# Kernel optimization log

Hardware: AMD Instinct MI355X
Metric: run time of the kernel (lower is better)

The kernel has to match this reference:

```python
import jax, jax.numpy as jnp
import numpy as np

B, S, D = 8, 1024, 1024
H, DH = 16, 64  # num_attention_heads, attention_head_size; H*DH == D


def setup_inputs() -> dict:
    key = jax.random.key(0)
    ks = jax.random.split(key, 6)
    scale = 0.02
    return {
        "hidden_states": jax.random.normal(ks[0], (B, S, D), jnp.float32),
        "right_hidden_states": jax.random.normal(ks[1], (B, S, D), jnp.float32),
        "attention_mask": jnp.ones((B, S, S), jnp.float32),
        "Wq": jax.random.normal(ks[2], (D, H * DH), jnp.float32) * scale,
        "bq": jnp.zeros((H * DH,), jnp.float32),
        "Wk": jax.random.normal(ks[3], (D, H * DH), jnp.float32) * scale,
        "bk": jnp.zeros((H * DH,), jnp.float32),
        "Wv": jax.random.normal(ks[4], (D, H * DH), jnp.float32) * scale,
        "bv": jnp.zeros((H * DH,), jnp.float32),
    }


def _split_heads(x, b):
    # (B, S, H*DH) -> (B, H, S, DH)
    return x.reshape(b, -1, H, DH).transpose(0, 2, 1, 3)


def reference(hidden_states, right_hidden_states, attention_mask, Wq, bq, Wk, bk, Wv, bv):
    b = hidden_states.shape[0]
    q = _split_heads(hidden_states @ Wq + bq, b)          # (B,H,Sq,DH)
    k = _split_heads(right_hidden_states @ Wk + bk, b)    # (B,H,Sk,DH)
    v = _split_heads(right_hidden_states @ Wv + bv, b)    # (B,H,Sk,DH)

    scores = jnp.einsum("bhqd,bhkd->bhqk", q, k) / jnp.sqrt(jnp.asarray(DH, q.dtype))
    scores = jnp.sum(scores, axis=1, keepdims=True)       # (B,1,Sq,Sk) head-summed

    ext = (1.0 - attention_mask[:, None, :, :].astype(scores.dtype)) * -1e9
    probs = jax.nn.softmax(scores + ext, axis=-1)         # (B,1,Sq,Sk)

    ctx = jnp.matmul(probs, v)                            # broadcast -> (B,H,Sq,DH)
    # Faithful to original: reshape WITHOUT transposing heads back.
    return ctx.reshape(b, -1, H * DH)                     # (B,Sq,H*DH)
```

## Files before the change

### kernel.cpp

```cpp
#include <hip/hip_runtime.h>
#include <stdint.h>

constexpr int S = 1024;
constexpr int D = 1024;
constexpr int NB = 8;

typedef __bf16 bf16x8 __attribute__((ext_vector_type(8)));
typedef float floatx4 __attribute__((ext_vector_type(4)));

#define AS1 __attribute__((address_space(1)))
#define AS3 __attribute__((address_space(3)))

__device__ __forceinline__ unsigned short f2bf(float f) {
  unsigned u = __builtin_bit_cast(unsigned, f);
  u += 0x7fffu + ((u >> 16) & 1u);
  return (unsigned short)(u >> 16);
}

__device__ __forceinline__ ushort4 f2bf4(float4 w) {
  ushort4 o;
  o.x = f2bf(w.x); o.y = f2bf(w.y); o.z = f2bf(w.z); o.w = f2bf(w.w);
  return o;
}

__device__ __forceinline__ void gload16(const void* g, void* l) {
  __builtin_amdgcn_global_load_lds((const AS1 unsigned int*)g, (AS3 unsigned int*)l, 16, 0, 0);
}

__global__ __launch_bounds__(256) void prep_kernel(
    const float4* __restrict__ hs4, const float4* __restrict__ rhs4,
    ushort4* __restrict__ hsb4, ushort4* __restrict__ rhsb4,
    const float* __restrict__ Wq, const float* __restrict__ Wk, const float* __restrict__ Wv,
    unsigned short* __restrict__ WvT, unsigned short* __restrict__ Mtb,
    const float* __restrict__ bq, const float* __restrict__ bk, float* __restrict__ u,
    float* __restrict__ v, float* __restrict__ cbuf) {
  __shared__ float tile[32][33];
  __shared__ float bsh[1024];
  __shared__ float sh[256];
  __shared__ int nz2;
  __shared__ __align__(16) unsigned short Am[64 * 32];
  __shared__ __align__(16) unsigned short Bm[64 * 32];
  const int bid = blockIdx.x;
  const int tid = threadIdx.x;
  if (bid < 256) {
    const int bx = bid & 15;
    const int by = bid >> 4;
    const int srow = tid >> 2;
    const int scg8 = (((tid & 3) ^ ((srow >> 1) & 3)) * 8);
    const int lw8 = (tid & 3) * 8;
    const float* aGp = Wk + (long long)(by * 64 + srow) * 1024 + scg8;
    const float* bGp = Wq + (long long)(bx * 64 + srow) * 1024 + scg8;
    const int lane = tid & 63;
    const int w4 = tid >> 6;
    const int r15 = lane & 15;
    const int quad = lane >> 4;
    const int pq = (quad ^ ((r15 >> 1) & 3)) * 8;
    const int wm2 = (w4 >> 1) * 32;
    const int wn2 = (w4 & 1) * 32;
    floatx4 acc[2][2];
    for (int i = 0; i < 2; ++i)
      for (int j = 0; j < 2; ++j) acc[i][j] = {0.f, 0.f, 0.f, 0.f};
    for (int k0 = 0; k0 < 1024; k0 += 32) {
      float4 a0 = *(const float4*)(aGp + k0);
      float4 a1 = *(const float4*)(aGp + k0 + 4);
      float4 b0 = *(const float4*)(bGp + k0);
      float4 b1 = *(const float4*)(bGp + k0 + 4);
      ushort4 ua0 = f2bf4(a0), ua1 = f2bf4(a1), ub0 = f2bf4(b0), ub1 = f2bf4(b1);
      __syncthreads();
      *(ushort4*)(Am + srow * 32 + lw8) = ua0;
      *(ushort4*)(Am + srow * 32 + lw8 + 4) = ua1;
      *(ushort4*)(Bm + srow * 32 + lw8) = ub0;
      *(ushort4*)(Bm + srow * 32 + lw8 + 4) = ub1;
      __syncthreads();
      bf16x8 af[2], bfr[2];
      for (int t = 0; t < 2; ++t) {
        af[t] = *reinterpret_cast<const bf16x8*>(Am + (wm2 + t * 16 + r15) * 32 + pq);
        bfr[t] = *reinterpret_cast<const bf16x8*>(Bm + (wn2 + t * 16 + r15) * 32 + pq);
      }
      for (int mt = 0; mt < 2; ++mt)
        for (int nt = 0; nt < 2; ++nt)
          acc[mt][nt] =
              __builtin_amdgcn_mfma_f32_16x16x32_bf16(af[mt], bfr[nt], acc[mt][nt], 0, 0, 0);
    }
    for (int mt = 0; mt < 2; ++mt)
      for (int nt = 0; nt < 2; ++nt) {
        const int mr = by * 64 + wm2 + mt * 16 + quad * 4;
        const int nc = bx * 64 + wn2 + nt * 16 + r15;
        floatx4 vv = acc[mt][nt];
        for (int e = 0; e < 4; ++e)
          Mtb[(long long)(mr + e) * 1024 + nc] = f2bf(vv[e] * 0.125f);
      }
  } else if (bid < 2304) {
    const int base = (bid - 256) * 256 + tid;
    float4 a0 = hs4[base];
    float4 a1 = hs4[base + 524288];
    float4 a2 = hs4[base + 1048576];
    float4 a3 = hs4[base + 1572864];
    float4 b0 = rhs4[base];
    float4 b1 = rhs4[base + 524288];
    float4 b2 = rhs4[base + 1048576];
    float4 b3 = rhs4[base + 1572864];
    hsb4[base] = f2bf4(a0);
    hsb4[base + 524288] = f2bf4(a1);
    hsb4[base + 1048576] = f2bf4(a2);
    hsb4[base + 1572864] = f2bf4(a3);
    rhsb4[base] = f2bf4(b0);
    rhsb4[base + 524288] = f2bf4(b1);
    rhsb4[base + 1048576] = f2bf4(b2);
    rhsb4[base + 1572864] = f2bf4(b3);
  } else if (bid < 3328) {
    const int r = bid - 2304;
    const int bx = (r & 31) * 32;
    const int by = (r >> 5) * 32;
    const int x = tid & 31;
    const int y0 = tid >> 5;
    for (int i = 0; i < 4; ++i) {
      int y = y0 + i * 8;
      tile[y][x] = Wv[(by + y) * D + bx + x];
    }
    __syncthreads();
    for (int i = 0; i < 4; ++i) {
      int y = y0 + i * 8;
      WvT[(long long)(bx + y) * D + by + x] = f2bf(tile[x][y]);
    }
  } else if (bid < 3336) {
    const bool isU = bid < 3332;
    const int blk = isU ? (bid - 3328) : (bid - 3332);
    const float* W = isU ? Wq : Wk;
    const float* bvec = isU ? bk : bq;
    float* outv = isU ? u : v;
    if (tid == 0) nz2 = 0;
    __syncthreads();
    float4 q = ((const float4*)bvec)[tid];
    bsh[tid * 4 + 0] = q.x;
    bsh[tid * 4 + 1] = q.y;
    bsh[tid * 4 + 2] = q.z;
    bsh[tid * 4 + 3] = q.w;
    if (q.x != 0.f || q.y != 0.f || q.z != 0.f || q.w != 0.f) nz2 = 1;
    __syncthreads();
    const int row0 = blk * 256;
    if (!nz2) {
      outv[row0 + tid] = 0.f;
      return;
    }
    const int lane = tid & 63;
    const int wv = tid >> 6;
    for (int rr = 0; rr < 64; ++rr) {
      const int row = row0 + wv * 64 + rr;
      const float* rp = W + (long long)row * 1024;
      float s = 0.f;
#pragma unroll
      for (int k = 0; k < 16; ++k) s += rp[lane + 64 * k] * bsh[lane + 64 * k];
      s += __shfl_xor(s, 32, 64);
      s += __shfl_xor(s, 16, 64);
      s += __shfl_xor(s, 8, 64);
      s += __shfl_xor(s, 4, 64);
      s += __shfl_xor(s, 2, 64);
      s += __shfl_xor(s, 1, 64);
      if (lane == 0) outv[row] = 0.125f * s;
    }
  } else {
    float s = 0.f;
    for (int c = tid; c < 1024; c += 256) s += bq[c] * bk[c];
    sh[tid] = s;
    __syncthreads();
    for (int o = 128; o; o >>= 1) {
      if (tid < o) sh[tid] += sh[tid + o];
      __syncthreads();
    }
    if (tid == 0) cbuf[0] = 0.125f * sh[0];
  }
}


#define GEMM_COMMON_IDX                  \
  const int tid = threadIdx.x;           \
  const int lane = tid & 63;             \
  const int w = tid >> 6;                \
  const int r15 = lane & 15;             \
  const int quad = lane >> 4;            \
  const int pq = (quad ^ ((r15 >> 1) & 3)) * 8; \
  const int wm = (w >> 1) * 64;          \
  const int wn = (w & 1) * 64;

#define GEMM_ACC_INIT                    \
  floatx4 acc[4][4];                     \
  for (int i = 0; i < 4; ++i)            \
    for (int j = 0; j < 4; ++j) acc[i][j] = {0.f, 0.f, 0.f, 0.f};

#define GEMM_STAGE_SETUP64(Abase, lda_, Bbase, ldb_)                          \
  const int srow = tid >> 2;                                                  \
  const int scg = (((tid & 3) ^ ((srow >> 1) & 3)) * 8);                      \
  const unsigned short* aG0 = (Abase) + (long long)srow * (lda_) + scg;       \
  const unsigned short* aG1 = aG0 + (long long)64 * (lda_);                   \
  const unsigned short* bG0 = (Bbase) + (long long)srow * (ldb_) + scg;       \
  const unsigned short* bG1 = bG0 + (long long)64 * (ldb_);

#define GEMM_KLOOP64(Klen)                                                               \
  for (int k0 = 0; k0 < (Klen); k0 += 64) {                                              \
    gload16(aG0 + k0, As[0] + w * 512);                                                  \
    gload16(aG1 + k0, As[0] + w * 512 + 2048);                                           \
    gload16(aG0 + k0 + 32, As[1] + w * 512);                                             \
    gload16(aG1 + k0 + 32, As[1] + w * 512 + 2048);                                      \
    gload16(bG0 + k0, Bs[0] + w * 512);                                                  \
    gload16(bG1 + k0, Bs[0] + w * 512 + 2048);                                           \
    gload16(bG0 + k0 + 32, Bs[1] + w * 512);                                             \
    gload16(bG1 + k0 + 32, Bs[1] + w * 512 + 2048);                                      \
    __syncthreads();                                                                     \
    for (int h = 0; h < 2; ++h) {                                                        \
      bf16x8 af[4], bfr[4];                                                              \
      for (int t = 0; t < 4; ++t) {                                                      \
        af[t] = *reinterpret_cast<const bf16x8*>(As[h] + (wm + t * 16 + r15) * 32 + pq); \
        bfr[t] = *reinterpret_cast<const bf16x8*>(Bs[h] + (wn + t * 16 + r15) * 32 + pq);\
      }                                                                                  \
      for (int mt = 0; mt < 4; ++mt)                                                     \
        for (int nt = 0; nt < 4; ++nt)                                                   \
          acc[mt][nt] =                                                                  \
              __builtin_amdgcn_mfma_f32_16x16x32_bf16(af[mt], bfr[nt], acc[mt][nt], 0, 0, 0); \
    }                                                                                    \
    __syncthreads();                                                                     \
  }

__global__ __launch_bounds__(256) void gemm_fused_kernel(
    const unsigned short* __restrict__ hsb, const unsigned short* __restrict__ rhsb,
    const unsigned short* __restrict__ Mtb, const unsigned short* __restrict__ WvT,
    const float* __restrict__ bv, unsigned short* __restrict__ hsMb,
    unsigned short* __restrict__ Vmt, const float* __restrict__ hs,
    const float* __restrict__ rhs, const float* __restrict__ u, const float* __restrict__ v,
    const float* __restrict__ cbuf, float* __restrict__ t2, float* __restrict__ t3) {
  __shared__ __align__(16) unsigned short As[2][4096];
  __shared__ __align__(16) unsigned short Bs[2][4096];
  GEMM_COMMON_IDX
  const int bid = blockIdx.x;
  if (bid >= 1024) {
    __shared__ int nz;
    const bool isT2 = bid < 1056;
    const int row = ((isT2 ? bid - 1024 : bid - 1056) << 8) + tid;
    const float* vec = isT2 ? u : v;
    const float* mat = isT2 ? hs : rhs;
    float* outp = isT2 ? t2 : t3;
    if (tid == 0) nz = 0;
    __syncthreads();
    float4 q = ((const float4*)vec)[tid];
    if (q.x != 0.f || q.y != 0.f || q.z != 0.f || q.w != 0.f) nz = 1;
    __syncthreads();
    const float c2 = 0.5f * cbuf[0];
    if (!nz) {
      outp[row] = c2;
      return;
    }
    const float4* r4 = (const float4*)(mat + (long long)row * 1024);
    float s = 0.f;
    for (int c4 = 0; c4 < 256; ++c4) {
      float4 h = r4[c4];
      s += h.x * vec[c4 * 4 + 0] + h.y * vec[c4 * 4 + 1] + h.z * vec[c4 * 4 + 2] +
           h.w * vec[c4 * 4 + 3];
    }
    outp[row] = s + c2;
    return;
  }
  const int swz = (bid & 7) * 128 + (bid >> 3);
  const int bx = swz & 15;
  const int by = swz >> 4;
  const int seg = bx >> 3;
  const long long nloc = (long long)(bx & 7) * 128;
  const long long m0 = (long long)by * 128;
  const unsigned short* A = ((seg == 0) ? hsb : rhsb) + m0 * D;
  const unsigned short* Bt = ((seg == 0) ? Mtb : WvT) + nloc * D;

  GEMM_STAGE_SETUP64(A, D, Bt, D)
  GEMM_ACC_INIT
  GEMM_KLOOP64(D)

  for (int mt = 0; mt < 4; ++mt) {
    for (int nt = 0; nt < 4; ++nt) {
      const long long mrow = m0 + wm + mt * 16 + quad * 4;
      const long long nc = nloc + wn + nt * 16 + r15;
      floatx4 vv = acc[mt][nt];
      if (seg == 0) {
        for (int e = 0; e < 4; ++e) hsMb[(mrow + e) * D + nc] = f2bf(vv[e]);
      } else {
        const float bval = bv[nc];
        for (int e = 0; e < 4; ++e) {
          long long m = mrow + e;
          Vmt[(m >> 10) * (long long)(S * D) + nc * S + (m & 1023)] = f2bf(vv[e] + bval);
        }
      }
    }
  }
}

__global__ __launch_bounds__(256) void gemm_scores_kernel(
    const unsigned short* __restrict__ hsMb, const unsigned short* __restrict__ rhsb,
    const float* __restrict__ mask, unsigned short* __restrict__ E, float* __restrict__ rowsumP,
    const float* __restrict__ t2, const float* __restrict__ t3) {
  __shared__ __align__(16) unsigned short As[2][4096];
  __shared__ __align__(16) unsigned short Bs[2][4096];
  GEMM_COMMON_IDX
  const int bid = blockIdx.x;
  const int z = bid & 7;
  const int r = bid >> 3;
  const int by = r >> 3;
  const int bx = r & 7;
  const long long m0 = (long long)by * 128;
  const long long n0 = (long long)bx * 128;
  const unsigned short* A = hsMb + (long long)z * S * D + m0 * D;
  const unsigned short* Bt = rhsb + (long long)z * S * D + n0 * D;

  GEMM_STAGE_SETUP64(A, D, Bt, D)
  GEMM_ACC_INIT
  GEMM_KLOOP64(D)

  const long long zE = (long long)z * S * 1024;
  float rowpart[4][4];
  for (int mt = 0; mt < 4; ++mt)
    for (int e = 0; e < 4; ++e) rowpart[mt][e] = 0.f;

  for (int mt = 0; mt < 4; ++mt) {
    for (int nt = 0; nt < 4; ++nt) {
      const long long mrow = m0 + wm + mt * 16 + quad * 4;
      const long long nc = n0 + wn + nt * 16 + r15;
      const float t3v = t3[z * 1024 + nc];
      floatx4 vv = acc[mt][nt];
      for (int e = 0; e < 4; ++e) {
        long long m = mrow + e;
        float mval = mask[zE + m * 1024 + nc];
        float sc = vv[e] + t2[z * 1024 + m] + t3v + (1.0f - mval) * -1e9f;
        float Ev = __expf(sc);
        E[zE + m * 1024 + nc] = f2bf(Ev);
        rowpart[mt][e] += Ev;
      }
    }
  }
  const int slot = (bx << 11) + ((wn >> 6) << 10);
  for (int mt = 0; mt < 4; ++mt) {
    for (int e = 0; e < 4; ++e) {
      float s = rowpart[mt][e];
      s += __shfl_xor(s, 1, 64);
      s += __shfl_xor(s, 2, 64);
      s += __shfl_xor(s, 4, 64);
      s += __shfl_xor(s, 8, 64);
      if (r15 == 0) {
        int mloc = (int)(m0 + wm + mt * 16 + quad * 4 + e);
        rowsumP[(z << 14) + slot + mloc] = s;
      }
    }
  }
}

__global__ __launch_bounds__(256) void gemm_ctx_kernel(const unsigned short* __restrict__ E,
                                                       const unsigned short* __restrict__ Vmt,
                                                       const float* __restrict__ rowsumP,
                                                       float* __restrict__ out) {
  __shared__ __align__(16) unsigned short As[2][4096];
  __shared__ __align__(16) unsigned short Bs[2][4096];
  __shared__ float rsinv[128];
  GEMM_COMMON_IDX
  const int bid = blockIdx.x;
  const int z = bid & 7;
  const int r = bid >> 3;
  const int by = r >> 3;
  const int bx = r & 7;
  const long long m0 = (long long)by * 128;
  const long long n0 = (long long)bx * 128;
  const unsigned short* A = E + (long long)z * S * 1024 + m0 * 1024;
  const unsigned short* Bt = Vmt + (long long)z * S * D + n0 * D;

  if (tid < 128) {
    float s = 0.f;
    for (int t = 0; t < 16; ++t) s += rowsumP[(z << 14) + (t << 10) + (int)m0 + tid];
    rsinv[tid] = 1.0f / s;
  }

  GEMM_STAGE_SETUP64(A, 1024, Bt, D)
  GEMM_ACC_INIT
  GEMM_KLOOP64(1024)

  for (int mt = 0; mt < 4; ++mt) {
    for (int nt = 0; nt < 4; ++nt) {
      const int r0 = wm + mt * 16 + quad * 4;
      const long long ncol = n0 + wn + nt * 16 + r15;
      floatx4 vv = acc[mt][nt];
      for (int e = 0; e < 4; ++e) {
        long long m = m0 + r0 + e;
        float val = vv[e] * rsinv[r0 + e];
        out[(long long)z * S * D + (ncol >> 6) * (long long)(S * 64) + m * 64 + (ncol & 63)] =
            val;
      }
    }
  }
}

extern "C" void kernel_launch(void* const* d_in, const int* in_sizes, int n_in, void* d_out,
                              int out_size, void* d_ws, size_t ws_size, hipStream_t stream) {
  const float* hs = (const float*)d_in[0];
  const float* rhs = (const float*)d_in[1];
  const float* mask = (const float*)d_in[2];
  const float* Wq = (const float*)d_in[3];
  const float* bq = (const float*)d_in[4];
  const float* Wk = (const float*)d_in[5];
  const float* bk = (const float*)d_in[6];
  const float* Wv = (const float*)d_in[7];
  const float* bv = (const float*)d_in[8];
  float* out = (float*)d_out;
  char* ws = (char*)d_ws;
  const size_t MB = 1ull << 20;
  unsigned short* WvT = (unsigned short*)(ws + 0 * MB);
  unsigned short* Mtb = (unsigned short*)(ws + 2 * MB);
  float* u = (float*)(ws + 8 * MB);
  float* v = (float*)(ws + 8 * MB + 4096);
  float* cbuf = (float*)(ws + 8 * MB + 8192);
  float* t2 = (float*)(ws + 8 * MB + 16384);
  float* t3 = (float*)(ws + 8 * MB + 49152);
  float* rowsumP = (float*)(ws + 8 * MB + 131072);
  unsigned short* hsb = (unsigned short*)(ws + 9 * MB);
  unsigned short* rhsb = (unsigned short*)(ws + 25 * MB);
  unsigned short* hsMb = (unsigned short*)(ws + 41 * MB);
  unsigned short* Vmt = (unsigned short*)(ws + 57 * MB);
  unsigned short* E = (unsigned short*)(ws + 9 * MB);

  prep_kernel<<<3337, 256, 0, stream>>>((const float4*)hs, (const float4*)rhs, (ushort4*)hsb,
                                        (ushort4*)rhsb, Wq, Wk, Wv, WvT, Mtb, bq, bk, u, v,
                                        cbuf);

  gemm_fused_kernel<<<1088, 256, 0, stream>>>(hsb, rhsb, Mtb, WvT, bv, hsMb, Vmt, hs, rhs, u,
                                              v, cbuf, t2, t3);

  gemm_scores_kernel<<<512, 256, 0, stream>>>(hsMb, rhsb, mask, E, rowsumP, t2, t3);

  gemm_ctx_kernel<<<512, 256, 0, stream>>>(E, Vmt, rowsumP, out);
}
```

Before: 267.1 us.

## Fuse fp32-to-bf16 activation conversion into GEMM operand loads

Removes the separate prep-stage pass that converted hidden_states and right_hidden_states to bf16. The GEMM kernels now read fp32 activations directly, pack them to bf16 in registers and write them to LDS, while the other operand keeps using async global-to-LDS loads. This saves a full read and write of two large activation tensors, at the cost of twice the global read bytes per GEMM tile, register-staged stores and extra conversion ALU work inside the k-loop. rhs is now read as fp32 by both the fused and scores GEMMs, and the workspace layout is compacted.

```diff
diff --git a/kernel.cpp b/kernel.cpp
--- a/kernel.cpp
+++ b/kernel.cpp
@@ -7,6 +7,7 @@
 
 typedef __bf16 bf16x8 __attribute__((ext_vector_type(8)));
 typedef float floatx4 __attribute__((ext_vector_type(4)));
+typedef unsigned short ushort8v __attribute__((ext_vector_type(8)));
 
 #define AS1 __attribute__((address_space(1)))
 #define AS3 __attribute__((address_space(3)))
@@ -23,13 +24,18 @@
   return o;
 }
 
+__device__ __forceinline__ ushort8v pack8(float4 a, float4 b) {
+  ushort8v r;
+  r[0] = f2bf(a.x); r[1] = f2bf(a.y); r[2] = f2bf(a.z); r[3] = f2bf(a.w);
+  r[4] = f2bf(b.x); r[5] = f2bf(b.y); r[6] = f2bf(b.z); r[7] = f2bf(b.w);
+  return r;
+}
+
 __device__ __forceinline__ void gload16(const void* g, void* l) {
   __builtin_amdgcn_global_load_lds((const AS1 unsigned int*)g, (AS3 unsigned int*)l, 16, 0, 0);
 }
 
 __global__ __launch_bounds__(256) void prep_kernel(
-    const float4* __restrict__ hs4, const float4* __restrict__ rhs4,
-    ushort4* __restrict__ hsb4, ushort4* __restrict__ rhsb4,
     const float* __restrict__ Wq, const float* __restrict__ Wk, const float* __restrict__ Wv,
     unsigned short* __restrict__ WvT, unsigned short* __restrict__ Mtb,
     const float* __restrict__ bq, const float* __restrict__ bk, float* __restrict__ u,
@@ -90,26 +96,8 @@
         for (int e = 0; e < 4; ++e)
           Mtb[(long long)(mr + e) * 1024 + nc] = f2bf(vv[e] * 0.125f);
       }
-  } else if (bid < 2304) {
-    const int base = (bid - 256) * 256 + tid;
-    float4 a0 = hs4[base];
-    float4 a1 = hs4[base + 524288];
-    float4 a2 = hs4[base + 1048576];
-    float4 a3 = hs4[base + 1572864];
-    float4 b0 = rhs4[base];
-    float4 b1 = rhs4[base + 524288];
-    float4 b2 = rhs4[base + 1048576];
-    float4 b3 = rhs4[base + 1572864];
-    hsb4[base] = f2bf4(a0);
-    hsb4[base + 524288] = f2bf4(a1);
-    hsb4[base + 1048576] = f2bf4(a2);
-    hsb4[base + 1572864] = f2bf4(a3);
-    rhsb4[base] = f2bf4(b0);
-    rhsb4[base + 524288] = f2bf4(b1);
-    rhsb4[base + 1048576] = f2bf4(b2);
-    rhsb4[base + 1572864] = f2bf4(b3);
-  } else if (bid < 3328) {
-    const int r = bid - 2304;
+  } else if (bid < 1280) {
+    const int r = bid - 256;
     const int bx = (r & 31) * 32;
     const int by = (r >> 5) * 32;
     const int x = tid & 31;
@@ -123,9 +111,9 @@
       int y = y0 + i * 8;
       WvT[(long long)(bx + y) * D + by + x] = f2bf(tile[x][y]);
     }
-  } else if (bid < 3336) {
-    const bool isU = bid < 3332;
-    const int blk = isU ? (bid - 3328) : (bid - 3332);
+  } else if (bid < 1288) {
+    const bool isU = bid < 1284;
+    const int blk = isU ? (bid - 1280) : (bid - 1284);
     const float* W = isU ? Wq : Wk;
     const float* bvec = isU ? bk : bq;
     float* outv = isU ? u : v;
@@ -188,6 +176,19 @@
   for (int i = 0; i < 4; ++i)            \
     for (int j = 0; j < 4; ++j) acc[i][j] = {0.f, 0.f, 0.f, 0.f};
 
+#define GEMM_COMPUTE64                                                                   \
+  for (int h = 0; h < 2; ++h) {                                                          \
+    bf16x8 af[4], bfr[4];                                                                \
+    for (int t = 0; t < 4; ++t) {                                                        \
+      af[t] = *reinterpret_cast<const bf16x8*>(As[h] + (wm + t * 16 + r15) * 32 + pq);   \
+      bfr[t] = *reinterpret_cast<const bf16x8*>(Bs[h] + (wn + t * 16 + r15) * 32 + pq);  \
+    }                                                                                    \
+    for (int mt = 0; mt < 4; ++mt)                                                       \
+      for (int nt = 0; nt < 4; ++nt)                                                     \
+        acc[mt][nt] =                                                                    \
+            __builtin_amdgcn_mfma_f32_16x16x32_bf16(af[mt], bfr[nt], acc[mt][nt], 0, 0, 0); \
+  }
+
 #define GEMM_STAGE_SETUP64(Abase, lda_, Bbase, ldb_)                          \
   const int srow = tid >> 2;                                                  \
   const int scg = (((tid & 3) ^ ((srow >> 1) & 3)) * 8);                      \
@@ -207,26 +208,79 @@
     gload16(bG0 + k0 + 32, Bs[1] + w * 512);                                             \
     gload16(bG1 + k0 + 32, Bs[1] + w * 512 + 2048);                                      \
     __syncthreads();                                                                     \
-    for (int h = 0; h < 2; ++h) {                                                        \
-      bf16x8 af[4], bfr[4];                                                              \
-      for (int t = 0; t < 4; ++t) {                                                      \
-        af[t] = *reinterpret_cast<const bf16x8*>(As[h] + (wm + t * 16 + r15) * 32 + pq); \
-        bfr[t] = *reinterpret_cast<const bf16x8*>(Bs[h] + (wn + t * 16 + r15) * 32 + pq);\
-      }                                                                                  \
-      for (int mt = 0; mt < 4; ++mt)                                                     \
-        for (int nt = 0; nt < 4; ++nt)                                                   \
-          acc[mt][nt] =                                                                  \
-              __builtin_amdgcn_mfma_f32_16x16x32_bf16(af[mt], bfr[nt], acc[mt][nt], 0, 0, 0); \
-    }                                                                                    \
+    GEMM_COMPUTE64                                                                       \
+    __syncthreads();                                                                     \
+  }
+
+#define GEMM_SETUP_AF32(Af32, lda_, Bbase, ldb_)                        \
+  const int srow = tid >> 2;                                            \
+  const int scg = (((tid & 3) ^ ((srow >> 1) & 3)) * 8);                \
+  const float* aF0 = (Af32) + (long long)srow * (lda_) + scg;           \
+  const float* aF1 = aF0 + (long long)64 * (lda_);                      \
+  const unsigned short* bG0 = (Bbase) + (long long)srow * (ldb_) + scg; \
+  const unsigned short* bG1 = bG0 + (long long)64 * (ldb_);             \
+  const int ldst = srow * 32 + (tid & 3) * 8;
+
+#define GEMM_KLOOP64_AF32(Klen)                                                          \
+  for (int k0 = 0; k0 < (Klen); k0 += 64) {                                              \
+    gload16(bG0 + k0, Bs[0] + w * 512);                                                  \
+    gload16(bG1 + k0, Bs[0] + w * 512 + 2048);                                           \
+    gload16(bG0 + k0 + 32, Bs[1] + w * 512);                                             \
+    gload16(bG1 + k0 + 32, Bs[1] + w * 512 + 2048);                                      \
+    float4 a00 = *(const float4*)(aF0 + k0);                                             \
+    float4 a01 = *(const float4*)(aF0 + k0 + 4);                                         \
+    float4 a10 = *(const float4*)(aF1 + k0);                                             \
+    float4 a11 = *(const float4*)(aF1 + k0 + 4);                                         \
+    float4 a20 = *(const float4*)(aF0 + k0 + 32);                                        \
+    float4 a21 = *(const float4*)(aF0 + k0 + 36);                                        \
+    float4 a30 = *(const float4*)(aF1 + k0 + 32);                                        \
+    float4 a31 = *(const float4*)(aF1 + k0 + 36);                                        \
+    *(ushort8v*)(As[0] + ldst) = pack8(a00, a01);                                        \
+    *(ushort8v*)(As[0] + 2048 + ldst) = pack8(a10, a11);                                 \
+    *(ushort8v*)(As[1] + ldst) = pack8(a20, a21);                                        \
+    *(ushort8v*)(As[1] + 2048 + ldst) = pack8(a30, a31);                                 \
+    __syncthreads();                                                                     \
+    GEMM_COMPUTE64                                                                       \
+    __syncthreads();                                                                     \
+  }
+
+#define GEMM_SETUP_BF32(Abase, lda_, Bf32, ldb_)                        \
+  const int srow = tid >> 2;                                            \
+  const int scg = (((tid & 3) ^ ((srow >> 1) & 3)) * 8);                \
+  const unsigned short* aG0 = (Abase) + (long long)srow * (lda_) + scg; \
+  const unsigned short* aG1 = aG0 + (long long)64 * (lda_);             \
+  const float* bF0 = (Bf32) + (long long)srow * (ldb_) + scg;           \
+  const float* bF1 = bF0 + (long long)64 * (ldb_);                      \
+  const int ldst = srow * 32 + (tid & 3) * 8;
+
+#define GEMM_KLOOP64_BF32(Klen)                                                          \
+  for (int k0 = 0; k0 < (Klen); k0 += 64) {                                              \
+    gload16(aG0 + k0, As[0] + w * 512);                                                  \
+    gload16(aG1 + k0, As[0] + w * 512 + 2048);                                           \
+    gload16(aG0 + k0 + 32, As[1] + w * 512);                                             \
+    gload16(aG1 + k0 + 32, As[1] + w * 512 + 2048);                                      \
+    float4 b00 = *(const float4*)(bF0 + k0);                                             \
+    float4 b01 = *(const float4*)(bF0 + k0 + 4);                                         \
+    float4 b10 = *(const float4*)(bF1 + k0);                                             \
+    float4 b11 = *(const float4*)(bF1 + k0 + 4);                                         \
+    float4 b20 = *(const float4*)(bF0 + k0 + 32);                                        \
+    float4 b21 = *(const float4*)(bF0 + k0 + 36);                                        \
+    float4 b30 = *(const float4*)(bF1 + k0 + 32);                                        \
+    float4 b31 = *(const float4*)(bF1 + k0 + 36);                                        \
+    *(ushort8v*)(Bs[0] + ldst) = pack8(b00, b01);                                        \
+    *(ushort8v*)(Bs[0] + 2048 + ldst) = pack8(b10, b11);                                 \
+    *(ushort8v*)(Bs[1] + ldst) = pack8(b20, b21);                                        \
+    *(ushort8v*)(Bs[1] + 2048 + ldst) = pack8(b30, b31);                                 \
+    __syncthreads();                                                                     \
+    GEMM_COMPUTE64                                                                       \
     __syncthreads();                                                                     \
   }
 
 __global__ __launch_bounds__(256) void gemm_fused_kernel(
-    const unsigned short* __restrict__ hsb, const unsigned short* __restrict__ rhsb,
+    const float* __restrict__ hs, const float* __restrict__ rhs,
     const unsigned short* __restrict__ Mtb, const unsigned short* __restrict__ WvT,
     const float* __restrict__ bv, unsigned short* __restrict__ hsMb,
-    unsigned short* __restrict__ Vmt, const float* __restrict__ hs,
-    const float* __restrict__ rhs, const float* __restrict__ u, const float* __restrict__ v,
+    unsigned short* __restrict__ Vmt, const float* __restrict__ u, const float* __restrict__ v,
     const float* __restrict__ cbuf, float* __restrict__ t2, float* __restrict__ t3) {
   __shared__ __align__(16) unsigned short As[2][4096];
   __shared__ __align__(16) unsigned short Bs[2][4096];
@@ -265,12 +319,12 @@
   const int seg = bx >> 3;
   const long long nloc = (long long)(bx & 7) * 128;
   const long long m0 = (long long)by * 128;
-  const unsigned short* A = ((seg == 0) ? hsb : rhsb) + m0 * D;
+  const float* Af = ((seg == 0) ? hs : rhs) + m0 * D;
   const unsigned short* Bt = ((seg == 0) ? Mtb : WvT) + nloc * D;
 
-  GEMM_STAGE_SETUP64(A, D, Bt, D)
+  GEMM_SETUP_AF32(Af, D, Bt, D)
   GEMM_ACC_INIT
-  GEMM_KLOOP64(D)
+  GEMM_KLOOP64_AF32(D)
 
   for (int mt = 0; mt < 4; ++mt) {
     for (int nt = 0; nt < 4; ++nt) {
@@ -291,7 +345,7 @@
 }
 
 __global__ __launch_bounds__(256) void gemm_scores_kernel(
-    const unsigned short* __restrict__ hsMb, const unsigned short* __restrict__ rhsb,
+    const unsigned short* __restrict__ hsMb, const float* __restrict__ rhs,
     const float* __restrict__ mask, unsigned short* __restrict__ E, float* __restrict__ rowsumP,
     const float* __restrict__ t2, const float* __restrict__ t3) {
   __shared__ __align__(16) unsigned short As[2][4096];
@@ -305,11 +359,11 @@
   const long long m0 = (long long)by * 128;
   const long long n0 = (long long)bx * 128;
   const unsigned short* A = hsMb + (long long)z * S * D + m0 * D;
-  const unsigned short* Bt = rhsb + (long long)z * S * D + n0 * D;
-
-  GEMM_STAGE_SETUP64(A, D, Bt, D)
+  const float* Bf = rhs + (long long)z * S * D + n0 * D;
+
+  GEMM_SETUP_BF32(A, D, Bf, D)
   GEMM_ACC_INIT
-  GEMM_KLOOP64(D)
+  GEMM_KLOOP64_BF32(D)
 
   const long long zE = (long long)z * S * 1024;
   float rowpart[4][4];
@@ -407,26 +461,22 @@
   const size_t MB = 1ull << 20;
   unsigned short* WvT = (unsigned short*)(ws + 0 * MB);
   unsigned short* Mtb = (unsigned short*)(ws + 2 * MB);
-  float* u = (float*)(ws + 8 * MB);
-  float* v = (float*)(ws + 8 * MB + 4096);
-  float* cbuf = (float*)(ws + 8 * MB + 8192);
-  float* t2 = (float*)(ws + 8 * MB + 16384);
-  float* t3 = (float*)(ws + 8 * MB + 49152);
-  float* rowsumP = (float*)(ws + 8 * MB + 131072);
-  unsigned short* hsb = (unsigned short*)(ws + 9 * MB);
-  unsigned short* rhsb = (unsigned short*)(ws + 25 * MB);
-  unsigned short* hsMb = (unsigned short*)(ws + 41 * MB);
-  unsigned short* Vmt = (unsigned short*)(ws + 57 * MB);
-  unsigned short* E = (unsigned short*)(ws + 9 * MB);
-
-  prep_kernel<<<3337, 256, 0, stream>>>((const float4*)hs, (const float4*)rhs, (ushort4*)hsb,
-                                        (ushort4*)rhsb, Wq, Wk, Wv, WvT, Mtb, bq, bk, u, v,
-                                        cbuf);
-
-  gemm_fused_kernel<<<1088, 256, 0, stream>>>(hsb, rhsb, Mtb, WvT, bv, hsMb, Vmt, hs, rhs, u,
-                                              v, cbuf, t2, t3);
-
-  gemm_scores_kernel<<<512, 256, 0, stream>>>(hsMb, rhsb, mask, E, rowsumP, t2, t3);
+  float* u = (float*)(ws + 4 * MB);
+  float* v = (float*)(ws + 4 * MB + 4096);
+  float* cbuf = (float*)(ws + 4 * MB + 8192);
+  float* t2 = (float*)(ws + 4 * MB + 16384);
+  float* t3 = (float*)(ws + 4 * MB + 49152);
+  float* rowsumP = (float*)(ws + 4 * MB + 131072);
+  unsigned short* hsMb = (unsigned short*)(ws + 5 * MB);
+  unsigned short* Vmt = (unsigned short*)(ws + 21 * MB);
+  unsigned short* E = (unsigned short*)(ws + 37 * MB);
+
+  prep_kernel<<<1289, 256, 0, stream>>>(Wq, Wk, Wv, WvT, Mtb, bq, bk, u, v, cbuf);
+
+  gemm_fused_kernel<<<1088, 256, 0, stream>>>(hs, rhs, Mtb, WvT, bv, hsMb, Vmt, u, v, cbuf,
+                                              t2, t3);
+
+  gemm_scores_kernel<<<512, 256, 0, stream>>>(hsMb, rhs, mask, E, rowsumP, t2, t3);
 
   gemm_ctx_kernel<<<512, 256, 0, stream>>>(E, Vmt, rowsumP, out);
 }
```

Measured after the change: 290.8 us. 1.09x slower.
